# Kernel tuning notes

Measured on AMD Instinct MI355X. Metric: run time of the kernel, lower is better.

Reference implementation:

```python
import jax, jax.numpy as jnp
import numpy as np

INPUT_SIZE = 512
HIDDEN_SIZE = 1024
OUTPUT_SIZE = 512

def _xavier(key, shape):
    fan_out, fan_in = shape
    limit = jnp.sqrt(6.0 / (fan_in + fan_out))
    return jax.random.uniform(key, shape, jnp.float32, -limit, limit)

def setup_inputs() -> dict:
    key = jax.random.key(0)
    ks = jax.random.split(key, 6)
    in_h = INPUT_SIZE + HIDDEN_SIZE
    x = jax.random.normal(ks[0], (128, 256, INPUT_SIZE), jnp.float32)
    return {
        "x": x,
        "W_f": _xavier(ks[1], (HIDDEN_SIZE, in_h)), "b_f": jnp.zeros((HIDDEN_SIZE,), jnp.float32),
        "W_i": _xavier(ks[2], (HIDDEN_SIZE, in_h)), "b_i": jnp.zeros((HIDDEN_SIZE,), jnp.float32),
        "W_c": _xavier(ks[3], (HIDDEN_SIZE, in_h)), "b_c": jnp.zeros((HIDDEN_SIZE,), jnp.float32),
        "W_o": _xavier(ks[4], (HIDDEN_SIZE, in_h)), "b_o": jnp.zeros((HIDDEN_SIZE,), jnp.float32),
        "W_out": _xavier(ks[5], (OUTPUT_SIZE, HIDDEN_SIZE)), "b_out": jnp.zeros((OUTPUT_SIZE,), jnp.float32),
    }

def reference(x, W_f, b_f, W_i, b_i, W_c, b_c, W_o, b_o, W_out, b_out):
    B = x.shape[0]
    H = W_f.shape[0]
    h0 = jnp.zeros((B, H), x.dtype)
    c0 = jnp.zeros((B, H), x.dtype)

    def step(carry, x_t):
        h, c = carry
        combined = jnp.concatenate([x_t, h], axis=1)  # [B, In+H]
        f = jax.nn.sigmoid(combined @ W_f.T + b_f)
        i = jax.nn.sigmoid(combined @ W_i.T + b_i)
        c_tilde = jnp.tanh(combined @ W_c.T + b_c)
        o = jax.nn.sigmoid(combined @ W_o.T + b_o)
        c_new = f * c + i * c_tilde
        h_new = o * jnp.tanh(c_new)
        return (h_new, c_new), h_new

    # scan over time: x transposed to [T, B, In]
    (_, _), hs = jax.lax.scan(step, (h0, c0), jnp.swapaxes(x, 0, 1))
    hs = jnp.swapaxes(hs, 0, 1)  # [B, T, H]
    outputs = jnp.einsum('bth,oh->bto', hs, W_out) + b_out
    return outputs
```

## Files before the change

kernel.cpp:

```cpp
#include <hip/hip_runtime.h>
#include <stdint.h>

#define B_   128
#define T_   256
#define IN_  512
#define H_   1024
#define NG_  4096
#define KC_  1536
#define OUT_ 512
#define NBLK 256
#define NTHR 512

typedef __bf16 bf16x8 __attribute__((ext_vector_type(8)));
typedef float  f32x4  __attribute__((ext_vector_type(4)));

__device__ __forceinline__ ushort f2bf(float f) {
    union { float f; uint32_t u; } v; v.f = f;
    uint32_t u = v.u;
    return (ushort)((u + 0x7FFFu + ((u >> 16) & 1u)) >> 16);
}

__device__ __forceinline__ f32x4 mfma16(bf16x8 a, bf16x8 b, f32x4 c) {
    return __builtin_amdgcn_mfma_f32_16x16x32_bf16(a, b, c, 0, 0, 0);
}

__device__ __forceinline__ float sigf(float x) {
    return 1.f / (1.f + __expf(-x));
}


__global__ void prep_w(const float* __restrict__ Wf, const float* __restrict__ Wi,
                       const float* __restrict__ Wc, const float* __restrict__ Wo,
                       ushort* __restrict__ Wcat) {
    int row = blockIdx.x;
    int j = row >> 2, g = row & 3;
    const float* W = (g == 0) ? Wf : (g == 1) ? Wi : (g == 2) ? Wc : Wo;
    for (int k = threadIdx.x; k < KC_; k += 256)
        Wcat[(size_t)row * KC_ + k] = f2bf(W[(size_t)j * KC_ + k]);
}

__global__ void prep_bias(const float* __restrict__ bf_, const float* __restrict__ bi_,
                          const float* __restrict__ bc_, const float* __restrict__ bo_,
                          float* __restrict__ bias) {
    int idx = blockIdx.x * 256 + threadIdx.x;
    int j = idx >> 2, g = idx & 3;
    const float* b = (g == 0) ? bf_ : (g == 1) ? bi_ : (g == 2) ? bc_ : bo_;
    bias[idx] = b[j];
}

__global__ void prep_wout(const float* __restrict__ W, ushort* __restrict__ Wb) {
    int row = blockIdx.x;
    for (int k = threadIdx.x; k < H_; k += 256)
        Wb[(size_t)row * H_ + k] = f2bf(W[(size_t)row * H_ + k]);
}

__global__ void prep_x(const float* __restrict__ x, ushort* __restrict__ xT) {
    int bid = blockIdx.x;
    int t = bid >> 7, b = bid & 127;
    const float* src = x  + ((size_t)b * T_ + t) * IN_;
    ushort*      dst = xT + ((size_t)t * B_ + b) * IN_;
    for (int k = threadIdx.x; k < IN_; k += 256) dst[k] = f2bf(src[k]);
}

__global__ void prep_zero(ushort* __restrict__ hs0, unsigned int* __restrict__ flags) {
    int idx = blockIdx.x * 256 + threadIdx.x;
    hs0[idx] = 0;
    if (idx < NBLK) flags[idx] = 0u;
}


__global__ void
__attribute__((amdgpu_flat_work_group_size(NTHR, NTHR), amdgpu_waves_per_eu(2, 2)))
lstm_persist(const ushort* __restrict__ xT,
             const ushort* __restrict__ Wcat,
             const float* __restrict__ bias,
             ushort* __restrict__ hs,
             unsigned int* flags)
{
    __shared__ ushort As[16 * 1536];

    const int tid  = threadIdx.x;
    const int lane = tid & 63;
    const int wv   = tid >> 6;
    const int bx   = blockIdx.x;
    const int grp  = bx & 7;
    const int sub  = bx >> 3;
    const int nbase = sub * 128;
    const int rbase = grp * 16;

    const int colg  = nbase + wv * 16 + (lane & 15);
    const int g     = lane & 3;
    const int unitg = colg >> 2;

    bf16x8 breg[48];
#pragma unroll
    for (int r = 0; r < 48; ++r)
        breg[r] = *(const bf16x8*)(Wcat + (size_t)colg * KC_ + r * 32 + (lane >> 4) * 8);
#pragma unroll
    for (int r = 0; r < 48; ++r) {
        f32x4 tmp = __builtin_bit_cast(f32x4, breg[r]);
        asm volatile("" : "+v"(tmp));
        breg[r] = __builtin_bit_cast(bf16x8, tmp);
    }

    const float biasv = bias[colg];
    float creg4[4] = {0.f, 0.f, 0.f, 0.f};

    const int srow = tid >> 5;
    const int sc32 = tid & 31;
    const int arow = lane & 15;

    for (int t = 0; t < T_; ++t) {
        const ushort* xTt = xT + ((size_t)t * B_ + rbase) * IN_;
        {
            uint4 v0 = *(const uint4*)(xTt + (size_t)srow * IN_ + sc32 * 8);
            uint4 v1 = *(const uint4*)(xTt + (size_t)srow * IN_ + (32 + sc32) * 8);
            *(uint4*)&As[srow * 1536 + ((sc32)      ^ (srow & 15)) * 8] = v0;
            *(uint4*)&As[srow * 1536 + ((32 + sc32) ^ (srow & 15)) * 8] = v1;
        }
        __syncthreads();

        f32x4 accs[2];
        accs[0] = (f32x4){0.f, 0.f, 0.f, 0.f};
        accs[1] = (f32x4){0.f, 0.f, 0.f, 0.f};
#pragma unroll
        for (int r = 0; r < 16; ++r) {
            const int s = r * 4 + (lane >> 4);
            bf16x8 a = *(const bf16x8*)&As[arow * 1536 + (s ^ (arow & 15)) * 8];
            accs[r & 1] = mfma16(a, breg[r], accs[r & 1]);
        }

        if (t > 0 && wv == 0) {
            const bool active = lane < 32;
            const unsigned int* fp = flags + (lane & 31) * 8 + grp;
            while (1) {
                unsigned v = active
                    ? __hip_atomic_load(fp, __ATOMIC_RELAXED, __HIP_MEMORY_SCOPE_AGENT)
                    : ~0u;
                if (__ballot(active && v < (unsigned)t) == 0ull) break;
                __builtin_amdgcn_s_sleep(1);
            }
        }
        __syncthreads();

        const unsigned int* hrow =
            (const unsigned int*)(hs + ((size_t)t * B_ + rbase + srow) * H_);
#pragma unroll
        for (int jb = 0; jb < 2; ++jb) {
            unsigned int hv[8];
#pragma unroll
            for (int j = 0; j < 8; ++j)
                hv[j] = __hip_atomic_load(hrow + (jb * 8 + j) * 32 + sc32,
                                          __ATOMIC_RELAXED, __HIP_MEMORY_SCOPE_AGENT);
#pragma unroll
            for (int j = 0; j < 8; ++j) {
                const int jj = jb * 8 + j;
                const int z = jj * 8 + (sc32 >> 2);
                *(unsigned int*)&As[srow * 1536 + ((64 + z) ^ (srow & 15)) * 8
                                    + (sc32 & 3) * 2] = hv[j];
            }
        }
        __syncthreads();

#pragma unroll
        for (int r = 16; r < 48; ++r) {
            const int s = r * 4 + (lane >> 4);
            bf16x8 a = *(const bf16x8*)&As[arow * 1536 + (s ^ (arow & 15)) * 8];
            accs[r & 1] = mfma16(a, breg[r], accs[r & 1]);
        }
        f32x4 acc = accs[0] + accs[1];

        unsigned int* hout = (unsigned int*)(hs + ((size_t)(t + 1) * B_ + rbase) * H_);
#pragma unroll
        for (int q = 0; q < 4; ++q) {
            float v = acc[q] + biasv;
            float a0 = (g == 2) ? tanhf(v) : sigf(v);
            float a1 = __shfl_xor(a0, 1);
            float a2 = __shfl_xor(a0, 2);
            float a3 = __shfl_xor(a1, 2);
            float vf = (g == 0) ? a0 : (g == 1) ? a1 : (g == 2) ? a2 : a3;
            float vi = (g == 0) ? a1 : (g == 1) ? a0 : (g == 2) ? a3 : a2;
            float vc = (g == 0) ? a2 : (g == 1) ? a3 : (g == 2) ? a0 : a1;
            float vo = (g == 0) ? a3 : (g == 1) ? a2 : (g == 2) ? a1 : a0;
            float cn = vf * creg4[q] + vi * vc;
            creg4[q] = cn;
            unsigned int hu = (unsigned int)f2bf(vo * tanhf(cn));
            unsigned int hp = (unsigned int)__shfl_xor((int)hu, 4);
            if ((lane & 7) == 0) {
                const int m = (lane >> 4) * 4 + q;
                __hip_atomic_store(hout + m * 512 + (unitg >> 1), hu | (hp << 16),
                                   __ATOMIC_RELAXED, __HIP_MEMORY_SCOPE_AGENT);
            }
        }
        __syncthreads();
        if (tid == 0)
            __hip_atomic_store(flags + bx, (unsigned)(t + 1), __ATOMIC_RELAXED,
                               __HIP_MEMORY_SCOPE_AGENT);
    }
}


__launch_bounds__(256, 2)
__global__ void out_gemm(const ushort* __restrict__ hsflat,
                         const ushort* __restrict__ Wout,
                         const float* __restrict__ bout,
                         float* __restrict__ out)
{
    __shared__ ushort As2[128 * 64];
    __shared__ ushort Bs2[64 * 64];
    const int tid  = threadIdx.x;
    const int lane = tid & 63;
    const int wave = tid >> 6;
    const int wm = (wave >> 1) * 64;
    const int wn = (wave & 1) * 32;
    const int mbase = (blockIdx.x >> 3) * 128;
    const int nbase = (blockIdx.x & 7) * 64;

    f32x4 acc[4][2];
#pragma unroll
    for (int i = 0; i < 4; i++)
#pragma unroll
        for (int j = 0; j < 2; j++) acc[i][j] = (f32x4){0.f, 0.f, 0.f, 0.f};

    for (int kc = 0; kc < H_ / 64; ++kc) {
        const int k0 = kc * 64;
        __syncthreads();
#pragma unroll
        for (int it = 0; it < 4; ++it) {
            int g = it * 256 + tid;
            int row = g >> 3;
            int seg = g & 7;
            uint4 v = *(const uint4*)(hsflat + (size_t)(mbase + row) * H_ + k0 + seg * 8);
            int dstg = seg ^ (row & 7);
            *(uint4*)&As2[row * 64 + dstg * 8] = v;
        }
#pragma unroll
        for (int it = 0; it < 2; ++it) {
            int g = it * 256 + tid;
            int row = g >> 3;
            int seg = g & 7;
            uint4 v = *(const uint4*)(Wout + (size_t)(nbase + row) * H_ + k0 + seg * 8);
            int dstg = seg ^ (row & 7);
            *(uint4*)&Bs2[row * 64 + dstg * 8] = v;
        }
        __syncthreads();
#pragma unroll
        for (int ks = 0; ks < 2; ++ks) {
            const int kg = ks * 4 + (lane >> 4);
            bf16x8 af[4], bfr[2];
#pragma unroll
            for (int mi = 0; mi < 4; ++mi) {
                int row = wm + mi * 16 + (lane & 15);
                int gi = kg ^ (row & 7);
                af[mi] = *(const bf16x8*)&As2[row * 64 + gi * 8];
            }
#pragma unroll
            for (int ni = 0; ni < 2; ++ni) {
                int row = wn + ni * 16 + (lane & 15);
                int gi = kg ^ (row & 7);
                bfr[ni] = *(const bf16x8*)&Bs2[row * 64 + gi * 8];
            }
#pragma unroll
            for (int mi = 0; mi < 4; ++mi)
#pragma unroll
                for (int ni = 0; ni < 2; ++ni)
                    acc[mi][ni] = mfma16(af[mi], bfr[ni], acc[mi][ni]);
        }
    }

#pragma unroll
    for (int mi = 0; mi < 4; ++mi) {
#pragma unroll
        for (int ni = 0; ni < 2; ++ni) {
            int col = nbase + wn + ni * 16 + (lane & 15);
            float bv = bout[col];
#pragma unroll
            for (int q = 0; q < 4; ++q) {
                int rt = mbase + wm + mi * 16 + (lane >> 4) * 4 + q;
                int b = rt & 127, tt = rt >> 7;
                out[((size_t)b * T_ + tt) * OUT_ + col] = acc[mi][ni][q] + bv;
            }
        }
    }
}


extern "C" void kernel_launch(void* const* d_in, const int* in_sizes, int n_in,
                              void* d_out, int out_size, void* d_ws, size_t ws_size,
                              hipStream_t stream)
{
    const float* x    = (const float*)d_in[0];
    const float* Wf   = (const float*)d_in[1];
    const float* bf_  = (const float*)d_in[2];
    const float* Wi   = (const float*)d_in[3];
    const float* bi_  = (const float*)d_in[4];
    const float* Wc   = (const float*)d_in[5];
    const float* bc_  = (const float*)d_in[6];
    const float* Wo   = (const float*)d_in[7];
    const float* bo_  = (const float*)d_in[8];
    const float* Wout = (const float*)d_in[9];
    const float* bout = (const float*)d_in[10];
    float* out = (float*)d_out;

    char* ws = (char*)d_ws;
    size_t off = 0;
    auto alloc = [&](size_t bytes) {
        char* p = ws + off;
        off += (bytes + 255) & ~(size_t)255;
        return p;
    };
    ushort* xT   = (ushort*)alloc((size_t)T_ * B_ * IN_ * 2);
    ushort* Wcat = (ushort*)alloc((size_t)NG_ * KC_ * 2);
    float*  bias = (float*) alloc((size_t)NG_ * 4);
    ushort* Wob  = (ushort*)alloc((size_t)OUT_ * H_ * 2);
    ushort* hs   = (ushort*)alloc((size_t)(T_ + 1) * B_ * H_ * 2);
    unsigned int* flags = (unsigned int*)alloc((size_t)NBLK * 4);

    hipLaunchKernelGGL(prep_w,    dim3(NG_), dim3(256), 0, stream, Wf, Wi, Wc, Wo, Wcat);
    hipLaunchKernelGGL(prep_bias, dim3(16),  dim3(256), 0, stream, bf_, bi_, bc_, bo_, bias);
    hipLaunchKernelGGL(prep_wout, dim3(OUT_),dim3(256), 0, stream, Wout, Wob);
    hipLaunchKernelGGL(prep_x,    dim3(T_ * B_), dim3(256), 0, stream, x, xT);
    hipLaunchKernelGGL(prep_zero, dim3(512), dim3(256), 0, stream, hs, flags);

    hipLaunchKernelGGL(lstm_persist, dim3(NBLK), dim3(NTHR), 0, stream,
                       xT, Wcat, bias, hs, flags);

    hipLaunchKernelGGL(out_gemm, dim3(2048), dim3(256), 0, stream,
                       hs + (size_t)B_ * H_, Wob, bout, out);
}
```

Baseline: 1.792 ms.

## Split LSTM recurrent GEMM K dimension across two wave halves with LDS reduction

Doubles the persistent LSTM block to 1024 threads and splits each column tile's K loop between two groups of 8 waves, interleaving K chunks. Each wave now holds 24 instead of 48 weight register fragments. The second half writes its partial sums to a shared scratch buffer and the first half reduces them before the gate nonlinearities. This is meant to halve the serial MFMA chain per step on the recurrent critical path. In exchange it adds an extra barrier and LDS round trip every step, and it changes the launch bounds and register budget.

```diff
diff --git a/kernel.cpp b/kernel.cpp
--- a/kernel.cpp
+++ b/kernel.cpp
@@ -9,7 +9,7 @@
 #define KC_  1536
 #define OUT_ 512
 #define NBLK 256
-#define NTHR 512
+#define NTHR 1024
 
 typedef __bf16 bf16x8 __attribute__((ext_vector_type(8)));
 typedef float  f32x4  __attribute__((ext_vector_type(4)));
@@ -69,8 +69,7 @@
 }
 
 
-__global__ void
-__attribute__((amdgpu_flat_work_group_size(NTHR, NTHR), amdgpu_waves_per_eu(2, 2)))
+__global__ void __launch_bounds__(NTHR, 4)
 lstm_persist(const ushort* __restrict__ xT,
              const ushort* __restrict__ Wcat,
              const float* __restrict__ bias,
@@ -78,26 +77,30 @@
              unsigned int* flags)
 {
     __shared__ ushort As[16 * 1536];
+    __shared__ float  scr[8][16][17];
 
     const int tid  = threadIdx.x;
     const int lane = tid & 63;
     const int wv   = tid >> 6;
+    const int nh   = wv & 7;
+    const int kh   = wv >> 3;
     const int bx   = blockIdx.x;
     const int grp  = bx & 7;
     const int sub  = bx >> 3;
     const int nbase = sub * 128;
     const int rbase = grp * 16;
 
-    const int colg  = nbase + wv * 16 + (lane & 15);
+    const int colg  = nbase + nh * 16 + (lane & 15);
     const int g     = lane & 3;
     const int unitg = colg >> 2;
 
-    bf16x8 breg[48];
-#pragma unroll
-    for (int r = 0; r < 48; ++r)
-        breg[r] = *(const bf16x8*)(Wcat + (size_t)colg * KC_ + r * 32 + (lane >> 4) * 8);
-#pragma unroll
-    for (int r = 0; r < 48; ++r) {
+    bf16x8 breg[24];
+#pragma unroll
+    for (int r = 0; r < 24; ++r)
+        breg[r] = *(const bf16x8*)(Wcat + (size_t)colg * KC_
+                                   + (2 * r + kh) * 32 + (lane >> 4) * 8);
+#pragma unroll
+    for (int r = 0; r < 24; ++r) {
         f32x4 tmp = __builtin_bit_cast(f32x4, breg[r]);
         asm volatile("" : "+v"(tmp));
         breg[r] = __builtin_bit_cast(bf16x8, tmp);
@@ -106,17 +109,15 @@
     const float biasv = bias[colg];
     float creg4[4] = {0.f, 0.f, 0.f, 0.f};
 
-    const int srow = tid >> 5;
-    const int sc32 = tid & 31;
+    const int srow = tid >> 6;
+    const int sc64 = tid & 63;
     const int arow = lane & 15;
 
     for (int t = 0; t < T_; ++t) {
         const ushort* xTt = xT + ((size_t)t * B_ + rbase) * IN_;
         {
-            uint4 v0 = *(const uint4*)(xTt + (size_t)srow * IN_ + sc32 * 8);
-            uint4 v1 = *(const uint4*)(xTt + (size_t)srow * IN_ + (32 + sc32) * 8);
-            *(uint4*)&As[srow * 1536 + ((sc32)      ^ (srow & 15)) * 8] = v0;
-            *(uint4*)&As[srow * 1536 + ((32 + sc32) ^ (srow & 15)) * 8] = v1;
+            uint4 vx = *(const uint4*)(xTt + (size_t)srow * IN_ + sc64 * 8);
+            *(uint4*)&As[srow * 1536 + (sc64 ^ (srow & 15)) * 8] = vx;
         }
         __syncthreads();
 
@@ -124,8 +125,8 @@
         accs[0] = (f32x4){0.f, 0.f, 0.f, 0.f};
         accs[1] = (f32x4){0.f, 0.f, 0.f, 0.f};
 #pragma unroll
-        for (int r = 0; r < 16; ++r) {
-            const int s = r * 4 + (lane >> 4);
+        for (int r = 0; r < 8; ++r) {
+            const int s = (2 * r + kh) * 4 + (lane >> 4);
             bf16x8 a = *(const bf16x8*)&As[arow * 1536 + (s ^ (arow & 15)) * 8];
             accs[r & 1] = mfma16(a, breg[r], accs[r & 1]);
         }
@@ -147,49 +148,59 @@
             (const unsigned int*)(hs + ((size_t)t * B_ + rbase + srow) * H_);
 #pragma unroll
         for (int jb = 0; jb < 2; ++jb) {
-            unsigned int hv[8];
-#pragma unroll
-            for (int j = 0; j < 8; ++j)
-                hv[j] = __hip_atomic_load(hrow + (jb * 8 + j) * 32 + sc32,
+            unsigned int hv[4];
+#pragma unroll
+            for (int j = 0; j < 4; ++j)
+                hv[j] = __hip_atomic_load(hrow + (jb * 4 + j) * 64 + sc64,
                                           __ATOMIC_RELAXED, __HIP_MEMORY_SCOPE_AGENT);
 #pragma unroll
-            for (int j = 0; j < 8; ++j) {
-                const int jj = jb * 8 + j;
-                const int z = jj * 8 + (sc32 >> 2);
+            for (int j = 0; j < 4; ++j) {
+                const int d = (jb * 4 + j) * 64 + sc64;
+                const int z = d >> 2;
                 *(unsigned int*)&As[srow * 1536 + ((64 + z) ^ (srow & 15)) * 8
-                                    + (sc32 & 3) * 2] = hv[j];
-            }
-        }
-        __syncthreads();
-
-#pragma unroll
-        for (int r = 16; r < 48; ++r) {
-            const int s = r * 4 + (lane >> 4);
+                                    + (d & 3) * 2] = hv[j];
+            }
+        }
+        __syncthreads();
+
+#pragma unroll
+        for (int r = 8; r < 24; ++r) {
+            const int s = (2 * r + kh) * 4 + (lane >> 4);
             bf16x8 a = *(const bf16x8*)&As[arow * 1536 + (s ^ (arow & 15)) * 8];
             accs[r & 1] = mfma16(a, breg[r], accs[r & 1]);
         }
         f32x4 acc = accs[0] + accs[1];
 
-        unsigned int* hout = (unsigned int*)(hs + ((size_t)(t + 1) * B_ + rbase) * H_);
-#pragma unroll
-        for (int q = 0; q < 4; ++q) {
-            float v = acc[q] + biasv;
-            float a0 = (g == 2) ? tanhf(v) : sigf(v);
-            float a1 = __shfl_xor(a0, 1);
-            float a2 = __shfl_xor(a0, 2);
-            float a3 = __shfl_xor(a1, 2);
-            float vf = (g == 0) ? a0 : (g == 1) ? a1 : (g == 2) ? a2 : a3;
-            float vi = (g == 0) ? a1 : (g == 1) ? a0 : (g == 2) ? a3 : a2;
-            float vc = (g == 0) ? a2 : (g == 1) ? a3 : (g == 2) ? a0 : a1;
-            float vo = (g == 0) ? a3 : (g == 1) ? a2 : (g == 2) ? a1 : a0;
-            float cn = vf * creg4[q] + vi * vc;
-            creg4[q] = cn;
-            unsigned int hu = (unsigned int)f2bf(vo * tanhf(cn));
-            unsigned int hp = (unsigned int)__shfl_xor((int)hu, 4);
-            if ((lane & 7) == 0) {
-                const int m = (lane >> 4) * 4 + q;
-                __hip_atomic_store(hout + m * 512 + (unitg >> 1), hu | (hp << 16),
-                                   __ATOMIC_RELAXED, __HIP_MEMORY_SCOPE_AGENT);
+        if (kh == 1) {
+#pragma unroll
+            for (int q = 0; q < 4; ++q)
+                scr[nh][(lane >> 4) * 4 + q][lane & 15] = acc[q];
+        }
+        __syncthreads();
+
+        if (kh == 0) {
+            unsigned int* hout =
+                (unsigned int*)(hs + ((size_t)(t + 1) * B_ + rbase) * H_);
+#pragma unroll
+            for (int q = 0; q < 4; ++q) {
+                const int row = (lane >> 4) * 4 + q;
+                float v = acc[q] + scr[nh][row][lane & 15] + biasv;
+                float a0 = (g == 2) ? tanhf(v) : sigf(v);
+                float a1 = __shfl_xor(a0, 1);
+                float a2 = __shfl_xor(a0, 2);
+                float a3 = __shfl_xor(a1, 2);
+                float vf = (g == 0) ? a0 : (g == 1) ? a1 : (g == 2) ? a2 : a3;
+                float vi = (g == 0) ? a1 : (g == 1) ? a0 : (g == 2) ? a3 : a2;
+                float vc = (g == 0) ? a2 : (g == 1) ? a3 : (g == 2) ? a0 : a1;
+                float vo = (g == 0) ? a3 : (g == 1) ? a2 : (g == 2) ? a1 : a0;
+                float cn = vf * creg4[q] + vi * vc;
+                creg4[q] = cn;
+                unsigned int hu = (unsigned int)f2bf(vo * tanhf(cn));
+                unsigned int hp = (unsigned int)__shfl_xor((int)hu, 4);
+                if ((lane & 7) == 0)
+                    __hip_atomic_store(hout + row * 512 + (unitg >> 1),
+                                       hu | (hp << 16),
+                                       __ATOMIC_RELAXED, __HIP_MEMORY_SCOPE_AGENT);
             }
         }
         __syncthreads();
```

Result: slower. 2.527 ms (+41.0%).
